# Kernel tuning notes

Hardware: AMD Instinct MI355X
Metric: run time of the kernel (lower is better)

Reference implementation:

```python
import jax, jax.numpy as jnp
import numpy as np
from jax import lax

B, T, D = 4, 4096, 1024  # d_inner == D (expansion=1.0)


def setup_inputs() -> dict:
    key = jax.random.key(0)
    ks = jax.random.split(key, 6)
    s = 1.0 / np.sqrt(D)  # xavier-ish scale
    return {
        "x": jax.random.normal(ks[0], (B, T, D), dtype=jnp.float32),
        "W_in": jax.random.normal(ks[1], (D, D), dtype=jnp.float32) * s,
        "W_alpha": jax.random.normal(ks[2], (D, D), dtype=jnp.float32) * s,
        "b_alpha": jnp.full((D,), 2.0, dtype=jnp.float32),
        "W_beta": jax.random.normal(ks[3], (D, D), dtype=jnp.float32) * s,
        "b_beta": jnp.zeros((D,), dtype=jnp.float32),
        "W_v": jax.random.normal(ks[4], (D, D), dtype=jnp.float32) * s,
        "b_v": jnp.zeros((D,), dtype=jnp.float32),
        "W_out": jax.random.normal(ks[5], (D, D), dtype=jnp.float32) * s,
    }


def reference(x, W_in, W_alpha, b_alpha, W_beta, b_beta, W_v, b_v, W_out):
    # x: [B, T, D]; torch nn.Linear convention y = x @ W.T
    xp = jax.nn.silu(jnp.einsum("btd,ed->bte", x, W_in))  # [B, T, Di]
    alpha = jax.nn.sigmoid(jnp.einsum("bte,fe->btf", xp, W_alpha) + b_alpha)
    beta = jax.nn.sigmoid(jnp.einsum("bte,fe->btf", xp, W_beta) + b_beta)
    v = jnp.tanh(jnp.einsum("bte,fe->btf", xp, W_v) + b_v)
    bv = beta * v  # precompute write term

    def step(h, ab):
        a_t, bv_t = ab  # each [B, Di]
        h = a_t * h + bv_t
        return h, h * jax.nn.silu(h)

    h0 = jnp.zeros((x.shape[0], W_alpha.shape[0]), dtype=x.dtype)
    h_last, outs = lax.scan(step, h0, (alpha.transpose(1, 0, 2), bv.transpose(1, 0, 2)))
    cell_out = outs.transpose(1, 0, 2)  # [B, T, Di]
    output = jnp.einsum("btf,df->btd", cell_out, W_out)
    return output, h_last
```

## Files before the change

kernel.cpp:

```cpp
#include <hip/hip_runtime.h>
#include <hip/hip_bf16.h>
#include <cstdint>
#include <cstddef>

typedef __bf16 bf16_t;
typedef _Float16 f16_t;
typedef __bf16 bf16x4 __attribute__((ext_vector_type(4)));
typedef __bf16 bf16x8 __attribute__((ext_vector_type(8)));
typedef float  f32x4  __attribute__((ext_vector_type(4)));
typedef float  f32x16 __attribute__((ext_vector_type(16)));

constexpr int kBatch = 4;
constexpr int kT = 4096;
constexpr int kD = 1024;
constexpr int kM = kBatch * kT;
constexpr int kCH = kBatch * kD;
constexpr int kNC = 128;
constexpr int kL  = kT / kNC;
constexpr int LDS_BYTES = 131072;

__device__ __forceinline__ size_t tiled_idx(int r, int c, int ktiles ) {
    return (size_t)((r >> 7) * ktiles + (c >> 6)) * 8192
         + (((r >> 5) & 3) << 11) + (((c >> 4) & 3) << 9)
         + (((c >> 3) & 1) << 8) + ((r & 31) << 3) + (c & 7);
}

__device__ __forceinline__ void async16(const bf16_t* g, char* l) {
    __builtin_amdgcn_global_load_lds(
        (const __attribute__((address_space(1))) uint32_t*)g,
        (__attribute__((address_space(3))) uint32_t*)l,
        16, 0, 0);
}

__device__ __forceinline__ float fast_sigmoid(float z) {
    return 1.f / (1.f + __expf(-z));
}
__device__ __forceinline__ float fast_tanh(float z) {
    z = fminf(10.f, fmaxf(-10.f, z));
    float e = __expf(2.f * z);
    return (e - 1.f) / (e + 1.f);
}

__global__ __launch_bounds__(256)
void cvt_tiled_kernel(const float* __restrict__ src, bf16_t* __restrict__ dst) {
    __shared__ __align__(16) bf16_t sl[8192];
    const int tile = blockIdx.x;
    const int rt = tile >> 4, kt = tile & 15;
    const int tid = threadIdx.x;
    const int c4 = tid & 15;
    const int rl0 = tid >> 4;
    const int coff = (((c4 >> 2) & 3) << 9) + (((c4 >> 1) & 1) << 8) + ((c4 & 1) << 2);
#pragma unroll
    for (int p = 0; p < 8; ++p) {
        const int r = p * 16 + rl0;
        float4 a = reinterpret_cast<const float4*>(src)[(size_t)(rt * 128 + r) * 256 + kt * 16 + c4];
        bf16x4 o;
        o[0] = (bf16_t)a.x; o[1] = (bf16_t)a.y; o[2] = (bf16_t)a.z; o[3] = (bf16_t)a.w;
        *reinterpret_cast<bf16x4*>(&sl[((r >> 5) << 11) + ((r & 31) << 3) + coff]) = o;
    }
    __syncthreads();
    bf16x8* d8 = reinterpret_cast<bf16x8*>(dst) + (size_t)tile * 1024;
    const bf16x8* s8 = reinterpret_cast<const bf16x8*>(sl);
#pragma unroll
    for (int j = 0; j < 4; ++j)
        d8[tid + j * 256] = s8[tid + j * 256];
}

template<int EPI>
__global__ __launch_bounds__(512, 2)
void gemm256(const bf16_t* __restrict__ A, const bf16_t* __restrict__ Bw,
             const float* __restrict__ bi0, const float* __restrict__ bi1,
             const float* __restrict__ bi2,
             void* __restrict__ out0, void* __restrict__ out1, void* __restrict__ out2,
             int M, int N, int K)
{
    extern __shared__ char lds[];
    const int tid  = threadIdx.x;
    const int lane = tid & 63;
    const int wv   = tid >> 6;
    const int wr   = wv >> 2;
    const int wc   = wv & 3;
    const int l32  = lane & 31;
    const int lh   = lane >> 5;

    int bid = blockIdx.y * gridDim.x + blockIdx.x;
    int nwg = gridDim.x * gridDim.y;
    int swz = (bid & 7) * (nwg >> 3) + (bid >> 3);
    int gx  = N >> 8;
    int n0  = (swz % gx) << 8;
    int m0  = (swz / gx) << 8;

    const int ktiles = K >> 6;
    const size_t g0 = (size_t)tid * 8, g1 = (size_t)(512 + tid) * 8;
    const int d0 = wv << 10, d1 = 8192 + (wv << 10);

    auto STAGE = [&](const bf16_t* G, int row0, int k0, int lds_base) {
        const bf16_t* base = G + (size_t)((row0 >> 7) * ktiles + (k0 >> 6)) * 8192;
        async16(base + g0, lds + lds_base + d0);
        async16(base + g1, lds + lds_base + d1);
    };
    auto STAGE_TILE = [&](int w, int bufo) {
        const int k0 = w << 6;
        STAGE(A,  m0,        k0, bufo);
        STAGE(A,  m0 + 128,  k0, bufo + 16384);
        STAGE(Bw, n0,        k0, bufo + 32768);
        STAGE(Bw, n0 + 128,  k0, bufo + 49152);
    };

    const int lane16 = lane << 4;
    int offA[4][4], offB[2][4];
#pragma unroll
    for (int m = 0; m < 4; ++m)
#pragma unroll
        for (int ks = 0; ks < 4; ++ks)
            offA[m][ks] = (m << 12) + (ks << 10) + lane16;
#pragma unroll
    for (int n = 0; n < 2; ++n)
#pragma unroll
        for (int ks = 0; ks < 4; ++ks)
            offB[n][ks] = ((((wc & 1) << 1) + n) << 12) + (ks << 10) + lane16;

    f32x16 acc[4][2];
#pragma unroll
    for (int i = 0; i < 4; ++i)
#pragma unroll
        for (int j = 0; j < 2; ++j)
            acc[i][j] = (f32x16)(0.f);

    const int NT = K >> 6;

    STAGE_TILE(0, 0);
    asm volatile("s_waitcnt vmcnt(0)" ::: "memory");
    asm volatile("s_barrier" ::: "memory");

    for (int w = 0; w < NT; ++w) {
        const int bufo  = (w & 1) << 16;
        const int nbufo = bufo ^ 65536;
        const int aReg = bufo + (wr << 14);
        const int bReg = bufo + 32768 + ((wc >> 1) << 14);

        if (w + 1 < NT) STAGE_TILE(w + 1, nbufo);

#pragma unroll
        for (int ks = 0; ks < 4; ++ks) {
            bf16x8 aF[4], bF[2];
#pragma unroll
            for (int m = 0; m < 4; ++m)
                aF[m] = *reinterpret_cast<const bf16x8*>(lds + aReg + offA[m][ks]);
#pragma unroll
            for (int n = 0; n < 2; ++n)
                bF[n] = *reinterpret_cast<const bf16x8*>(lds + bReg + offB[n][ks]);
            __builtin_amdgcn_s_setprio(1);
#pragma unroll
            for (int m = 0; m < 4; ++m)
#pragma unroll
                for (int n = 0; n < 2; ++n)
                    acc[m][n] = __builtin_amdgcn_mfma_f32_32x32x16_bf16(aF[m], bF[n], acc[m][n], 0, 0, 0);
            __builtin_amdgcn_s_setprio(0);
        }

        if (w + 1 < NT) {
            asm volatile("s_waitcnt vmcnt(0)" ::: "memory");
            asm volatile("s_barrier" ::: "memory");
        }
    }

    const int slab = n0 >> 10;
    const float* bia = (EPI == 4) ? (slab == 0 ? bi0 : slab == 1 ? bi1 : bi2) : nullptr;
#pragma unroll
    for (int nf = 0; nf < 2; ++nf) {
        const int colg = n0 + wc * 64 + nf * 32 + l32;
        const int cL = colg & (kD - 1);
        float bs = 0.f;
        if constexpr (EPI == 4) bs = bia[cL];
#pragma unroll
        for (int mf = 0; mf < 4; ++mf) {
            const int rbase = m0 + wr * 128 + mf * 32 + lh * 4;
#pragma unroll
            for (int rg = 0; rg < 16; ++rg) {
                const int rowg = rbase + (rg & 3) + ((rg >> 2) << 3);
                const float f = acc[mf][nf][rg];
                if constexpr (EPI == 0) {
                    float s = f * fast_sigmoid(f);
                    reinterpret_cast<bf16_t*>(out0)[tiled_idx(rowg, colg, N >> 6)] = (bf16_t)s;
                } else if constexpr (EPI == 3) {
                    __builtin_nontemporal_store(f, reinterpret_cast<float*>(out0) + (size_t)rowg * N + colg);
                } else {
                    const size_t idx = (size_t)rowg * kD + cL;
                    if (slab == 0) {
                        reinterpret_cast<f16_t*>(out0)[idx] = (f16_t)fast_sigmoid(f + bs);
                    } else if (slab == 1) {
                        reinterpret_cast<bf16_t*>(out1)[idx] = (bf16_t)fast_sigmoid(f + bs);
                    } else {
                        reinterpret_cast<bf16_t*>(out2)[idx] = (bf16_t)fast_tanh(f + bs);
                    }
                }
            }
        }
    }
}

__global__ void scan_chunk_kernel(const f16_t* __restrict__ alpha,
                                  const bf16_t* __restrict__ beta,
                                  const bf16_t* __restrict__ vv,
                                  float* __restrict__ Aagg,
                                  float* __restrict__ Bagg)
{
    const int u  = blockIdx.x * blockDim.x + threadIdx.x;
    const int ch = u & (kCH - 1);
    const int c  = u >> 12;
    const int b  = ch >> 10;
    const int d  = ch & (kD - 1);
    size_t base = ((size_t)b * kT + (size_t)c * kL) * kD + d;
    float Ac = 1.f, Bc = 0.f;
#pragma unroll 4
    for (int t = 0; t < kL; ++t) {
        float a  = (float)alpha[base];
        float bv = (float)beta[base] * (float)vv[base];
        Ac *= a;
        Bc = a * Bc + bv;
        base += kD;
    }
    Aagg[u] = Ac;
    Bagg[u] = Bc;
}

__global__ void scan_mid_kernel(const float* __restrict__ Aagg,
                                const float* __restrict__ Bagg,
                                float* __restrict__ Hin,
                                float* __restrict__ hlast)
{
    const int ch = blockIdx.x * blockDim.x + threadIdx.x;
    float h = 0.f;
#pragma unroll 8
    for (int c = 0; c < kNC; ++c) {
        Hin[(size_t)c * kCH + ch] = h;
        h = Aagg[(size_t)c * kCH + ch] * h + Bagg[(size_t)c * kCH + ch];
    }
    hlast[ch] = h;
}

__global__ void scan_out_kernel(const f16_t* __restrict__ alpha,
                                const bf16_t* __restrict__ beta,
                                const bf16_t* __restrict__ vv,
                                const float* __restrict__ Hin,
                                bf16_t* __restrict__ cell)
{
    const int u  = blockIdx.x * blockDim.x + threadIdx.x;
    const int ch = u & (kCH - 1);
    const int c  = u >> 12;
    const int b  = ch >> 10;
    const int d  = ch & (kD - 1);
    size_t base = ((size_t)b * kT + (size_t)c * kL) * kD + d;
    const int rt = b * 32 + (c >> 2);
    const int mb = (b * 128 + c) & 3;
    const size_t tb = (size_t)(rt * 16 + (d >> 6)) * 8192
                    + ((size_t)mb << 11) + (((d >> 4) & 3) << 9)
                    + (((d >> 3) & 1) << 8) + (d & 7);
    float h = Hin[u];
#pragma unroll 4
    for (int t = 0; t < kL; ++t) {
        float a  = (float)alpha[base];
        float bv = (float)beta[base] * (float)vv[base];
        h = a * h + bv;
        float s = 1.f / (1.f + __expf(-h));
        cell[tb + t * 8] = (bf16_t)(h * h * s);
        base += kD;
    }
}

extern "C" void kernel_launch(void* const* d_in, const int* in_sizes, int n_in,
                              void* d_out, int out_size, void* d_ws, size_t ws_size,
                              hipStream_t stream)
{
    const float* x     = (const float*)d_in[0];
    const float* W_in  = (const float*)d_in[1];
    const float* W_al  = (const float*)d_in[2];
    const float* b_al  = (const float*)d_in[3];
    const float* W_be  = (const float*)d_in[4];
    const float* b_be  = (const float*)d_in[5];
    const float* W_v   = (const float*)d_in[6];
    const float* b_v   = (const float*)d_in[7];
    const float* W_out = (const float*)d_in[8];

    float* out   = (float*)d_out;
    float* hlast = out + (size_t)kM * kD;

    char* ws = (char*)d_ws;
    size_t off = 0;
    auto alloc = [&](size_t bytes) -> void* {
        void* p = ws + off;
        off += (bytes + 255) & ~(size_t)255;
        return p;
    };
    bf16_t* xbf   = (bf16_t*)alloc((size_t)kM * kD * 2);
    bf16_t* xp    = (bf16_t*)alloc((size_t)kM * kD * 2);
    f16_t*  alpha = (f16_t*) alloc((size_t)kM * kD * 2);
    bf16_t* betab = (bf16_t*)alloc((size_t)kM * kD * 2);
    bf16_t* vb    = (bf16_t*)alloc((size_t)kM * kD * 2);
    bf16_t* wbf   = (bf16_t*)alloc((size_t)5 * kD * kD * 2);

    bf16_t* Winb = wbf;
    bf16_t* Wfus = wbf + 1 * (size_t)kD * kD;
    bf16_t* Wob  = wbf + 4 * (size_t)kD * kD;

    bf16_t* cell = xbf;
    float*  Aagg = (float*)xp;
    float*  Bagg = Aagg + (size_t)kNC * kCH;
    float*  Hin  = Bagg + (size_t)kNC * kCH;

    hipFuncSetAttribute(reinterpret_cast<const void*>(gemm256<0>), hipFuncAttributeMaxDynamicSharedMemorySize, LDS_BYTES);
    hipFuncSetAttribute(reinterpret_cast<const void*>(gemm256<3>), hipFuncAttributeMaxDynamicSharedMemorySize, LDS_BYTES);
    hipFuncSetAttribute(reinterpret_cast<const void*>(gemm256<4>), hipFuncAttributeMaxDynamicSharedMemorySize, LDS_BYTES);

    cvt_tiled_kernel<<<kM / 128 * 16, 256, 0, stream>>>(x, xbf);
    cvt_tiled_kernel<<<kD / 128 * 16, 256, 0, stream>>>(W_in,  Winb);
    cvt_tiled_kernel<<<kD / 128 * 16, 256, 0, stream>>>(W_al,  wbf + 1 * (size_t)kD * kD);
    cvt_tiled_kernel<<<kD / 128 * 16, 256, 0, stream>>>(W_be,  wbf + 2 * (size_t)kD * kD);
    cvt_tiled_kernel<<<kD / 128 * 16, 256, 0, stream>>>(W_v,   wbf + 3 * (size_t)kD * kD);
    cvt_tiled_kernel<<<kD / 128 * 16, 256, 0, stream>>>(W_out, Wob);

    dim3 grid1(kD / 256, kM / 256);
    dim3 gridF(3 * kD / 256, kM / 256);

    gemm256<0><<<grid1, 512, LDS_BYTES, stream>>>(xbf, Winb, nullptr, nullptr, nullptr,
                                                  xp, nullptr, nullptr, kM, kD, kD);
    gemm256<4><<<gridF, 512, LDS_BYTES, stream>>>(xp, Wfus, b_al, b_be, b_v,
                                                  alpha, betab, vb, kM, 3 * kD, kD);
    scan_chunk_kernel<<<kNC * kCH / 256, 256, 0, stream>>>(alpha, betab, vb, Aagg, Bagg);
    scan_mid_kernel<<<kCH / 256, 256, 0, stream>>>(Aagg, Bagg, Hin, hlast);
    scan_out_kernel<<<kNC * kCH / 256, 256, 0, stream>>>(alpha, betab, vb, Hin, cell);

    gemm256<3><<<grid1, 512, LDS_BYTES, stream>>>(cell, Wob, nullptr, nullptr, nullptr,
                                                  out, nullptr, nullptr, kM, kD, kD);
}
```

Baseline: 324.8 us.

## Switch GEMM to K=32 tiles with 4-stage async LDS pipeline; fuse conversions

Changes the tiled bf16 layout from 128x64 to 128x32 blocks and rewrites the GEMM main loop as a four-buffer pipeline. Three tiles stay in flight, waits use partial vmcnt counts, and there is one barrier per iteration instead of a full drain after each K step. The scan output and the EPI 0 epilogue are updated to write the new layout. The six fp32-to-bf16 conversion launches become one kernel that writes straight to global without an LDS staging buffer. The aim is to hide global load latency and cut launch overhead, at the cost of more barriers per unit of K and smaller MFMA batches per sync.

```diff
diff --git a/kernel.cpp b/kernel.cpp
--- a/kernel.cpp
+++ b/kernel.cpp
@@ -7,7 +7,6 @@
 typedef _Float16 f16_t;
 typedef __bf16 bf16x4 __attribute__((ext_vector_type(4)));
 typedef __bf16 bf16x8 __attribute__((ext_vector_type(8)));
-typedef float  f32x4  __attribute__((ext_vector_type(4)));
 typedef float  f32x16 __attribute__((ext_vector_type(16)));
 
 constexpr int kBatch = 4;
@@ -19,9 +18,9 @@
 constexpr int kL  = kT / kNC;
 constexpr int LDS_BYTES = 131072;
 
-__device__ __forceinline__ size_t tiled_idx(int r, int c, int ktiles ) {
-    return (size_t)((r >> 7) * ktiles + (c >> 6)) * 8192
-         + (((r >> 5) & 3) << 11) + (((c >> 4) & 3) << 9)
+__device__ __forceinline__ size_t tidx(int r, int c, int ntc) {
+    return (size_t)((r >> 7) * ntc + (c >> 5)) * 4096
+         + (((r >> 5) & 3) << 10) + (((c >> 4) & 1) << 9)
          + (((c >> 3) & 1) << 8) + ((r & 31) << 3) + (c & 7);
 }
 
@@ -42,28 +41,36 @@
 }
 
 __global__ __launch_bounds__(256)
-void cvt_tiled_kernel(const float* __restrict__ src, bf16_t* __restrict__ dst) {
-    __shared__ __align__(16) bf16_t sl[8192];
-    const int tile = blockIdx.x;
-    const int rt = tile >> 4, kt = tile & 15;
-    const int tid = threadIdx.x;
-    const int c4 = tid & 15;
-    const int rl0 = tid >> 4;
-    const int coff = (((c4 >> 2) & 3) << 9) + (((c4 >> 1) & 1) << 8) + ((c4 & 1) << 2);
-#pragma unroll
-    for (int p = 0; p < 8; ++p) {
-        const int r = p * 16 + rl0;
-        float4 a = reinterpret_cast<const float4*>(src)[(size_t)(rt * 128 + r) * 256 + kt * 16 + c4];
+void cvt2_kernel(const float* __restrict__ x,
+                 const float* __restrict__ w0, const float* __restrict__ w1,
+                 const float* __restrict__ w2, const float* __restrict__ w3,
+                 const float* __restrict__ w4,
+                 bf16_t* __restrict__ xd, bf16_t* __restrict__ wd)
+{
+    int tile = blockIdx.x;
+    const float* src; bf16_t* dst; int loc;
+    if (tile < 4096) { src = x; dst = xd; loc = tile; }
+    else {
+        int seg = (tile - 4096) >> 8;
+        loc = (tile - 4096) & 255;
+        src = seg == 0 ? w0 : seg == 1 ? w1 : seg == 2 ? w2 : seg == 3 ? w3 : w4;
+        dst = wd + (size_t)seg * kD * kD;
+    }
+    const int rt = loc >> 5, ct = loc & 31;
+    const int t = threadIdx.x;
+    const int c4 = t & 7;
+    const int r0 = t >> 3;
+    bf16_t* db = dst + (size_t)loc * 4096
+               + (((c4 >> 2) & 1) << 9) + (((c4 >> 1) & 1) << 8)
+               + (r0 << 3) + ((c4 & 1) << 2);
+#pragma unroll
+    for (int j = 0; j < 4; ++j) {
+        const int r = r0 + j * 32;
+        float4 a = reinterpret_cast<const float4*>(src)[(size_t)(rt * 128 + r) * 256 + ct * 8 + c4];
         bf16x4 o;
         o[0] = (bf16_t)a.x; o[1] = (bf16_t)a.y; o[2] = (bf16_t)a.z; o[3] = (bf16_t)a.w;
-        *reinterpret_cast<bf16x4*>(&sl[((r >> 5) << 11) + ((r & 31) << 3) + coff]) = o;
-    }
-    __syncthreads();
-    bf16x8* d8 = reinterpret_cast<bf16x8*>(dst) + (size_t)tile * 1024;
-    const bf16x8* s8 = reinterpret_cast<const bf16x8*>(sl);
-#pragma unroll
-    for (int j = 0; j < 4; ++j)
-        d8[tid + j * 256] = s8[tid + j * 256];
+        *reinterpret_cast<bf16x4*>(db + (j << 10)) = o;
+    }
 }
 
 template<int EPI>
@@ -90,35 +97,36 @@
     int n0  = (swz % gx) << 8;
     int m0  = (swz / gx) << 8;
 
-    const int ktiles = K >> 6;
-    const size_t g0 = (size_t)tid * 8, g1 = (size_t)(512 + tid) * 8;
-    const int d0 = wv << 10, d1 = 8192 + (wv << 10);
-
-    auto STAGE = [&](const bf16_t* G, int row0, int k0, int lds_base) {
-        const bf16_t* base = G + (size_t)((row0 >> 7) * ktiles + (k0 >> 6)) * 8192;
-        async16(base + g0, lds + lds_base + d0);
-        async16(base + g1, lds + lds_base + d1);
+    const int ntcK = K >> 5;
+    const size_t rstride = (size_t)ntcK * 4096;
+    const size_t atile0 = (size_t)(m0 >> 7) * rstride;
+    const size_t atile1 = atile0 + rstride;
+    const size_t btile0 = (size_t)(n0 >> 7) * rstride;
+    const size_t btile1 = btile0 + rstride;
+    const size_t g = (size_t)tid * 8;
+    const int tid16 = tid << 4;
+
+    auto STAGE_TILE = [&](int w, int bufo) {
+        const size_t kt = (size_t)w * 4096;
+        async16(A  + atile0 + kt + g, lds + bufo + tid16);
+        async16(A  + atile1 + kt + g, lds + bufo + 8192  + tid16);
+        async16(Bw + btile0 + kt + g, lds + bufo + 16384 + tid16);
+        async16(Bw + btile1 + kt + g, lds + bufo + 24576 + tid16);
     };
-    auto STAGE_TILE = [&](int w, int bufo) {
-        const int k0 = w << 6;
-        STAGE(A,  m0,        k0, bufo);
-        STAGE(A,  m0 + 128,  k0, bufo + 16384);
-        STAGE(Bw, n0,        k0, bufo + 32768);
-        STAGE(Bw, n0 + 128,  k0, bufo + 49152);
-    };
 
     const int lane16 = lane << 4;
-    int offA[4][4], offB[2][4];
-#pragma unroll
-    for (int m = 0; m < 4; ++m)
-#pragma unroll
-        for (int ks = 0; ks < 4; ++ks)
-            offA[m][ks] = (m << 12) + (ks << 10) + lane16;
-#pragma unroll
-    for (int n = 0; n < 2; ++n)
-#pragma unroll
-        for (int ks = 0; ks < 4; ++ks)
-            offB[n][ks] = ((((wc & 1) << 1) + n) << 12) + (ks << 10) + lane16;
+    const int aRegO = wr << 13;
+    const int bRegO = 16384 + ((wc >> 1) << 13);
+    int offA[2][4], offB[2][2];
+#pragma unroll
+    for (int ks = 0; ks < 2; ++ks) {
+#pragma unroll
+        for (int m = 0; m < 4; ++m)
+            offA[ks][m] = aRegO + (m << 11) + (ks << 10) + lane16;
+#pragma unroll
+        for (int n = 0; n < 2; ++n)
+            offB[ks][n] = bRegO + ((((wc & 1) << 1) + n) << 11) + (ks << 10) + lane16;
+    }
 
     f32x16 acc[4][2];
 #pragma unroll
@@ -127,42 +135,40 @@
         for (int j = 0; j < 2; ++j)
             acc[i][j] = (f32x16)(0.f);
 
-    const int NT = K >> 6;
+    const int NT = K >> 5;
 
     STAGE_TILE(0, 0);
-    asm volatile("s_waitcnt vmcnt(0)" ::: "memory");
-    asm volatile("s_barrier" ::: "memory");
+    STAGE_TILE(1, 32768);
+    STAGE_TILE(2, 65536);
 
     for (int w = 0; w < NT; ++w) {
-        const int bufo  = (w & 1) << 16;
-        const int nbufo = bufo ^ 65536;
-        const int aReg = bufo + (wr << 14);
-        const int bReg = bufo + 32768 + ((wc >> 1) << 14);
-
-        if (w + 1 < NT) STAGE_TILE(w + 1, nbufo);
-
-#pragma unroll
-        for (int ks = 0; ks < 4; ++ks) {
-            bf16x8 aF[4], bF[2];
+        const int bufo = (w & 3) << 15;
+        if (w + 2 < NT)      { asm volatile("s_waitcnt vmcnt(8)" ::: "memory"); }
+        else if (w + 1 < NT) { asm volatile("s_waitcnt vmcnt(4)" ::: "memory"); }
+        else                 { asm volatile("s_waitcnt vmcnt(0)" ::: "memory"); }
+        asm volatile("s_barrier" ::: "memory");
+
+        bf16x8 aF[2][4], bF[2][2];
+#pragma unroll
+        for (int ks = 0; ks < 2; ++ks) {
 #pragma unroll
             for (int m = 0; m < 4; ++m)
-                aF[m] = *reinterpret_cast<const bf16x8*>(lds + aReg + offA[m][ks]);
+                aF[ks][m] = *reinterpret_cast<const bf16x8*>(lds + bufo + offA[ks][m]);
 #pragma unroll
             for (int n = 0; n < 2; ++n)
-                bF[n] = *reinterpret_cast<const bf16x8*>(lds + bReg + offB[n][ks]);
-            __builtin_amdgcn_s_setprio(1);
+                bF[ks][n] = *reinterpret_cast<const bf16x8*>(lds + bufo + offB[ks][n]);
+        }
+        if (w + 3 < NT) STAGE_TILE(w + 3, ((w + 3) & 3) << 15);
+
+        __builtin_amdgcn_s_setprio(1);
+#pragma unroll
+        for (int ks = 0; ks < 2; ++ks)
 #pragma unroll
             for (int m = 0; m < 4; ++m)
 #pragma unroll
                 for (int n = 0; n < 2; ++n)
-                    acc[m][n] = __builtin_amdgcn_mfma_f32_32x32x16_bf16(aF[m], bF[n], acc[m][n], 0, 0, 0);
-            __builtin_amdgcn_s_setprio(0);
-        }
-
-        if (w + 1 < NT) {
-            asm volatile("s_waitcnt vmcnt(0)" ::: "memory");
-            asm volatile("s_barrier" ::: "memory");
-        }
+                    acc[m][n] = __builtin_amdgcn_mfma_f32_32x32x16_bf16(aF[ks][m], bF[ks][n], acc[m][n], 0, 0, 0);
+        __builtin_amdgcn_s_setprio(0);
     }
 
     const int slab = n0 >> 10;
@@ -182,7 +188,7 @@
                 const float f = acc[mf][nf][rg];
                 if constexpr (EPI == 0) {
                     float s = f * fast_sigmoid(f);
-                    reinterpret_cast<bf16_t*>(out0)[tiled_idx(rowg, colg, N >> 6)] = (bf16_t)s;
+                    reinterpret_cast<bf16_t*>(out0)[tidx(rowg, colg, N >> 5)] = (bf16_t)s;
                 } else if constexpr (EPI == 3) {
                     __builtin_nontemporal_store(f, reinterpret_cast<float*>(out0) + (size_t)rowg * N + colg);
                 } else {
@@ -252,10 +258,8 @@
     const int b  = ch >> 10;
     const int d  = ch & (kD - 1);
     size_t base = ((size_t)b * kT + (size_t)c * kL) * kD + d;
-    const int rt = b * 32 + (c >> 2);
-    const int mb = (b * 128 + c) & 3;
-    const size_t tb = (size_t)(rt * 16 + (d >> 6)) * 8192
-                    + ((size_t)mb << 11) + (((d >> 4) & 3) << 9)
+    const size_t tb = (size_t)((b * 32 + (c >> 2)) * 32 + (d >> 5)) * 4096
+                    + ((size_t)(c & 3) << 10) + (((d >> 4) & 1) << 9)
                     + (((d >> 3) & 1) << 8) + (d & 7);
     float h = Hin[u];
 #pragma unroll 4
@@ -313,12 +317,8 @@
     hipFuncSetAttribute(reinterpret_cast<const void*>(gemm256<3>), hipFuncAttributeMaxDynamicSharedMemorySize, LDS_BYTES);
     hipFuncSetAttribute(reinterpret_cast<const void*>(gemm256<4>), hipFuncAttributeMaxDynamicSharedMemorySize, LDS_BYTES);
 
-    cvt_tiled_kernel<<<kM / 128 * 16, 256, 0, stream>>>(x, xbf);
-    cvt_tiled_kernel<<<kD / 128 * 16, 256, 0, stream>>>(W_in,  Winb);
-    cvt_tiled_kernel<<<kD / 128 * 16, 256, 0, stream>>>(W_al,  wbf + 1 * (size_t)kD * kD);
-    cvt_tiled_kernel<<<kD / 128 * 16, 256, 0, stream>>>(W_be,  wbf + 2 * (size_t)kD * kD);
-    cvt_tiled_kernel<<<kD / 128 * 16, 256, 0, stream>>>(W_v,   wbf + 3 * (size_t)kD * kD);
-    cvt_tiled_kernel<<<kD / 128 * 16, 256, 0, stream>>>(W_out, Wob);
+    cvt2_kernel<<<4096 + 5 * 256, 256, 0, stream>>>(x, W_in, W_al, W_be, W_v, W_out,
+                                                    xbf, wbf);
 
     dim3 grid1(kD / 256, kM / 256);
     dim3 gridF(3 * kD / 256, kM / 256);
```

Result: no change. 329.9 us (+1.6%).
